# Optimization experiments

Hardware: AMD Instinct MI355X
Metric: run time of the kernel (lower is better)

The kernel has to match this reference:

```python
import jax, jax.numpy as jnp
import numpy as np

NUM_BANDS = 64
LATENT = 256
HIDDEN = 512
G = 8
K = 1024
GD = LATENT // G  # 32
BETA = 0.25


def setup_inputs() -> dict:
    key = jax.random.key(0)
    ks = jax.random.split(key, 10)
    B, T = 16, 1000
    bands = jax.random.normal(ks[0], (B, T, NUM_BANDS), dtype=jnp.float32)
    s = 0.02
    enc_w1 = jax.random.normal(ks[1], (NUM_BANDS, HIDDEN), dtype=jnp.float32) * s
    enc_b1 = jnp.zeros((HIDDEN,), dtype=jnp.float32)
    enc_w2 = jax.random.normal(ks[2], (HIDDEN, LATENT), dtype=jnp.float32) * s
    enc_b2 = jnp.zeros((LATENT,), dtype=jnp.float32)
    codebooks = jax.random.normal(ks[3], (G, K, GD), dtype=jnp.float32) * 0.1
    dec_w1 = jax.random.normal(ks[4], (LATENT, HIDDEN), dtype=jnp.float32) * s
    dec_b1 = jnp.zeros((HIDDEN,), dtype=jnp.float32)
    dec_w2 = jax.random.normal(ks[5], (HIDDEN, NUM_BANDS), dtype=jnp.float32) * s
    dec_b2 = jnp.zeros((NUM_BANDS,), dtype=jnp.float32)
    return {
        "bands": bands,
        "enc_w1": enc_w1, "enc_b1": enc_b1, "enc_w2": enc_w2, "enc_b2": enc_b2,
        "codebooks": codebooks,
        "dec_w1": dec_w1, "dec_b1": dec_b1, "dec_w2": dec_w2, "dec_b2": dec_b2,
    }


def _mlp(x, w1, b1, w2, b2):
    # TimeDistributedMLP: Linear -> ReLU -> Linear applied on last dim
    return jax.nn.relu(x @ w1 + b1) @ w2 + b2


def reference(bands, enc_w1, enc_b1, enc_w2, enc_b2, codebooks,
              dec_w1, dec_b1, dec_w2, dec_b2):
    B, T, _ = bands.shape
    z_e = _mlp(bands, enc_w1, enc_b1, enc_w2, enc_b2)  # (B,T,LATENT)

    # Grouped VQ over flattened frames
    parts = z_e.reshape(B * T, G, GD)                   # (N,G,gd)
    zn = jnp.sum(parts * parts, axis=-1)[:, :, None]    # (N,G,1)
    cn = jnp.sum(codebooks * codebooks, axis=-1)[None]  # (1,G,K)
    cross = jnp.einsum('ngd,gkd->ngk', parts, codebooks)
    dist = zn - 2.0 * cross + cn                        # (N,G,K)
    idx = jnp.argmin(dist, axis=-1)                     # (N,G) int
    z_q = codebooks[jnp.arange(G)[None, :], idx]        # (N,G,gd) gather

    # straight-through estimator
    z_q_st = parts + jax.lax.stop_gradient(z_q - parts)

    # per-group mean losses, summed over groups
    codebook_loss = jnp.sum(jnp.mean((jax.lax.stop_gradient(z_q) - parts) ** 2, axis=(0, 2)))
    commit_loss = jnp.sum(jnp.mean((z_q - jax.lax.stop_gradient(parts)) ** 2, axis=(0, 2)))
    vq_loss = BETA * (codebook_loss + commit_loss)  # epoch=None -> beta_eff = beta

    z_q_out = z_q_st.reshape(B, T, LATENT)
    idx_out = idx.reshape(B, T, G)
    bands_hat = _mlp(z_q_out, dec_w1, dec_b1, dec_w2, dec_b2)
    return (bands_hat, z_e, z_q_out, idx_out, vq_loss)
```

## Files before the change

kernel.cpp:

```cpp
#include <hip/hip_runtime.h>

#define NBANDS 64
#define LATENT 256
#define HIDDEN 512
#define GQ 8
#define KQ 1024
#define GD 32
#define NROWS 16000

#define OUT_BH   0
#define OUT_ZE   1024000
#define OUT_ZQ   5120000
#define OUT_IDX  9216000
#define OUT_LOSS 9344000

#define WS_H     0
#define WS_H2BF_F  0
#define WS_ZQB_F   4096000
#define WS_W1B_F   6144000
#define WS_W2B_F   6209536
#define WS_CN    8192000
#define WS_LOSS  8200192

typedef __attribute__((ext_vector_type(8))) short bf16x8;
typedef __attribute__((ext_vector_type(4))) float f32x4;

__device__ __forceinline__ unsigned short f2bf(float f) {
  unsigned u = __builtin_bit_cast(unsigned, f);
  unsigned r = u + 0x7FFFu + ((u >> 16) & 1u);
  return (unsigned short)(r >> 16);
}

__device__ __forceinline__ void g2l16(const float* g, float* l) {
  __builtin_amdgcn_global_load_lds(
      (const __attribute__((address_space(1))) unsigned int*)g,
      (__attribute__((address_space(3))) unsigned int*)l, 16, 0, 0);
}

template<int BN, int TM, int TN, int BK, bool RELU>
__global__ __launch_bounds__(256) void gemm_f32(
    const float* __restrict__ A, const float* __restrict__ B,
    const float* __restrict__ bias, float* __restrict__ C,
    int M, int N, int K) {
  constexpr int BM = 128;
  constexpr int NTX = BN / TN;
  constexpr int AF4 = BK / 8;
  constexpr int QPR = BN / 4;
  constexpr int BF4 = BK * BN / 1024;

  __shared__ float As[BK][BM + 8];
  __shared__ float Bs[BK][BN + 4];

  const int tid = threadIdx.x;
  const int tx = tid % NTX;
  const int ty = tid / NTX;
  const int row0 = blockIdx.y * BM;
  const int col0 = blockIdx.x * BN;

  const int arow = tid >> 1;
  const int akq  = (tid & 1) * (BK / 2);

  float acc[TM][TN] = {};

  for (int k0 = 0; k0 < K; k0 += BK) {
    float4 av[AF4], bv[BF4];
#pragma unroll
    for (int q = 0; q < AF4; ++q)
      av[q] = *reinterpret_cast<const float4*>(
          &A[(size_t)(row0 + arow) * K + k0 + akq + q * 4]);
#pragma unroll
    for (int t = 0; t < BF4; ++t) {
      const int qq = tid * BF4 + t;
      const int bk = qq / QPR, bn4 = qq % QPR;
      bv[t] = *reinterpret_cast<const float4*>(
          &B[(size_t)(k0 + bk) * N + col0 + bn4 * 4]);
    }
    __syncthreads();
#pragma unroll
    for (int q = 0; q < AF4; ++q) {
      As[akq + q * 4 + 0][arow] = av[q].x;
      As[akq + q * 4 + 1][arow] = av[q].y;
      As[akq + q * 4 + 2][arow] = av[q].z;
      As[akq + q * 4 + 3][arow] = av[q].w;
    }
#pragma unroll
    for (int t = 0; t < BF4; ++t) {
      const int qq = tid * BF4 + t;
      const int bk = qq / QPR, bn4 = qq % QPR;
      *reinterpret_cast<float4*>(&Bs[bk][bn4 * 4]) = bv[t];
    }
    __syncthreads();

#pragma unroll
    for (int kk = 0; kk < BK; ++kk) {
      float a[TM], b[TN];
#pragma unroll
      for (int q = 0; q < TM / 4; ++q) {
        float4 v = *reinterpret_cast<const float4*>(&As[kk][ty * TM + q * 4]);
        a[q * 4 + 0] = v.x; a[q * 4 + 1] = v.y;
        a[q * 4 + 2] = v.z; a[q * 4 + 3] = v.w;
      }
#pragma unroll
      for (int q = 0; q < TN / 4; ++q) {
        float4 v = *reinterpret_cast<const float4*>(&Bs[kk][tx * TN + q * 4]);
        b[q * 4 + 0] = v.x; b[q * 4 + 1] = v.y;
        b[q * 4 + 2] = v.z; b[q * 4 + 3] = v.w;
      }
#pragma unroll
      for (int i = 0; i < TM; ++i)
#pragma unroll
        for (int j = 0; j < TN; ++j)
          acc[i][j] = fmaf(a[i], b[j], acc[i][j]);
    }
  }

  float bb[TN];
#pragma unroll
  for (int q = 0; q < TN / 4; ++q) {
    float4 v = *reinterpret_cast<const float4*>(&bias[col0 + tx * TN + q * 4]);
    bb[q * 4 + 0] = v.x; bb[q * 4 + 1] = v.y;
    bb[q * 4 + 2] = v.z; bb[q * 4 + 3] = v.w;
  }
#pragma unroll
  for (int i = 0; i < TM; ++i) {
    const int r = row0 + ty * TM + i;
#pragma unroll
    for (int q = 0; q < TN / 4; ++q) {
      float4 v;
      float* vp = &v.x;
#pragma unroll
      for (int j = 0; j < 4; ++j) {
        float t = acc[i][q * 4 + j] + bb[q * 4 + j];
        if (RELU) t = fmaxf(t, 0.0f);
        vp[j] = t;
      }
      *reinterpret_cast<float4*>(&C[(size_t)r * N + col0 + tx * TN + q * 4]) = v;
    }
  }
}

template<int WM, bool OUT_BF16, bool DO_LOSS>
__global__ __launch_bounds__(256) void gemm_bf16_mfma(
    const unsigned short* __restrict__ A, const unsigned short* __restrict__ BT,
    const float* __restrict__ bias, void* __restrict__ Cout,
    int M, int N, int K,
    const float* __restrict__ loss_acc, float* __restrict__ loss_out) {
  constexpr int BM = 4 * WM;
  constexpr int MT = WM / 16;

  __shared__ unsigned short As[BM][40];
  __shared__ unsigned short Bs[64][40];

  const int tid  = threadIdx.x;
  const int wave = tid >> 6;
  const int lane = tid & 63;
  const int quad = lane >> 4;
  const int l16  = lane & 15;
  const int row0 = blockIdx.y * BM;
  const int col0 = blockIdx.x * 64;

  if (DO_LOSS && blockIdx.x == 0 && blockIdx.y == 0 && tid == 0)
    loss_out[0] = 0.5f * loss_acc[0] / (float)((size_t)NROWS * GD);

  f32x4 acc[MT][4];
#pragma unroll
  for (int mt = 0; mt < MT; ++mt)
#pragma unroll
    for (int nt = 0; nt < 4; ++nt) acc[mt][nt] = (f32x4){0.f, 0.f, 0.f, 0.f};

  for (int k0 = 0; k0 < K; k0 += 32) {
    __syncthreads();
    if constexpr (BM == 128) {
      const int r = tid >> 1, seg = (tid & 1) * 16;
      const uint4* src = reinterpret_cast<const uint4*>(
          &A[(size_t)(row0 + r) * K + k0 + seg]);
      uint4* dst = reinterpret_cast<uint4*>(&As[r][seg]);
      dst[0] = src[0]; dst[1] = src[1];
    } else {
      const int r = tid >> 2, seg = (tid & 3) * 8;
      *reinterpret_cast<uint4*>(&As[r][seg]) =
          *reinterpret_cast<const uint4*>(&A[(size_t)(row0 + r) * K + k0 + seg]);
    }
    {
      const int n = tid >> 2, kc = (tid & 3) * 8;
      *reinterpret_cast<uint4*>(&Bs[n][kc]) =
          *reinterpret_cast<const uint4*>(&BT[(size_t)(col0 + n) * K + k0 + kc]);
    }
    __syncthreads();

    bf16x8 af[MT], bf[4];
#pragma unroll
    for (int mt = 0; mt < MT; ++mt)
      af[mt] = *reinterpret_cast<const bf16x8*>(
          &As[wave * WM + mt * 16 + l16][quad * 8]);
#pragma unroll
    for (int nt = 0; nt < 4; ++nt)
      bf[nt] = *reinterpret_cast<const bf16x8*>(&Bs[nt * 16 + l16][quad * 8]);
#pragma unroll
    for (int mt = 0; mt < MT; ++mt)
#pragma unroll
      for (int nt = 0; nt < 4; ++nt)
        acc[mt][nt] = __builtin_amdgcn_mfma_f32_16x16x32_bf16(
            af[mt], bf[nt], acc[mt][nt], 0, 0, 0);
  }

#pragma unroll
  for (int mt = 0; mt < MT; ++mt)
#pragma unroll
    for (int nt = 0; nt < 4; ++nt) {
      const int col = col0 + nt * 16 + l16;
      const float bv = bias[col];
#pragma unroll
      for (int r = 0; r < 4; ++r) {
        const int grow = row0 + wave * WM + mt * 16 + quad * 4 + r;
        float v = acc[mt][nt][r] + bv;
        if constexpr (OUT_BF16) {
          v = fmaxf(v, 0.0f);
          ((unsigned short*)Cout)[(size_t)grow * N + col] = f2bf(v);
        } else {
          ((float*)Cout)[(size_t)grow * N + col] = v;
        }
      }
    }
}

__global__ void prep_cn(const float* __restrict__ cb, float* __restrict__ cn,
                        float* __restrict__ loss_acc) {
  const int i = blockIdx.x * 256 + threadIdx.x;
  if (i == 0) loss_acc[0] = 0.0f;
  if (i < GQ * KQ) {
    const float* c = cb + (size_t)i * GD;
    float s = 0.0f;
#pragma unroll
    for (int d = 0; d < GD; ++d) s = fmaf(c[d], c[d], s);
    cn[i] = s;
  }
}

__global__ void prep_wT(const float* __restrict__ w1, const float* __restrict__ w2,
                        unsigned short* __restrict__ w1bT,
                        unsigned short* __restrict__ w2bT) {
  const int t = blockIdx.x * 256 + threadIdx.x;
  if (t < 16384) {
    const int n = t >> 5, k0 = (t & 31) * 8;
    alignas(16) unsigned short o[8];
#pragma unroll
    for (int q = 0; q < 8; ++q) o[q] = f2bf(w1[(size_t)(k0 + q) * HIDDEN + n]);
    *reinterpret_cast<uint4*>(&w1bT[(size_t)n * LATENT + k0]) =
        *reinterpret_cast<const uint4*>(o);
  } else if (t < 20480) {
    const int u = t - 16384;
    const int n = u >> 6, k0 = (u & 63) * 8;
    alignas(16) unsigned short o[8];
#pragma unroll
    for (int q = 0; q < 8; ++q) o[q] = f2bf(w2[(size_t)(k0 + q) * NBANDS + n]);
    *reinterpret_cast<uint4*>(&w2bT[(size_t)n * HIDDEN + k0]) =
        *reinterpret_cast<const uint4*>(o);
  }
}

#define VQ_ROWS 128
#define VQ_CHUNK 128
#define VQ_NCHUNK (KQ / VQ_CHUNK)
#define ZPAD 36

__global__ __launch_bounds__(256) void vq_kernel(
    const float* __restrict__ z_e, const float* __restrict__ cb,
    const float* __restrict__ cn, float* __restrict__ z_q,
    unsigned short* __restrict__ zqb,
    float* __restrict__ idx_out, float* __restrict__ loss_acc) {
  const int g    = blockIdx.y;
  const int row0 = blockIdx.x * VQ_ROWS;
  const int tid  = threadIdx.x;
  const int tx   = tid & 15;
  const int ty   = tid >> 4;

  __shared__ float smem[VQ_ROWS * ZPAD + 2 * VQ_CHUNK * GD];
  float* zs  = smem;
  float* cbF = smem + VQ_ROWS * ZPAD;

  const float* cbg = cb + (size_t)g * KQ * GD;
  const float* cng = cn + (size_t)g * KQ;

  {
    const float* src = cbg;
    float* dst = cbF;
#pragma unroll
    for (int q4 = 0; q4 < 4; ++q4) {
      const int s = q4 * 256 + tid;
      const int r = s >> 3;
      const int q = (s & 7) ^ (r & 7);
      g2l16(src + r * GD + q * 4, dst + s * 4);
    }
  }

  {
    const int r   = tid >> 1;
    const int off = (tid & 1) << 4;
    const int key = ((r >> 3) & 3) << 2;
    const float4* src = reinterpret_cast<const float4*>(
        &z_e[(size_t)(row0 + r) * LATENT + g * GD + off]);
#pragma unroll
    for (int q = 0; q < 4; ++q)
      *reinterpret_cast<float4*>(&zs[r * ZPAD + ((off + q * 4) ^ key)]) = src[q];
  }

  const int akey = (ty & 3) << 2;
  const int bkey = tx & 7;

  float best[8];
  int   bidx[8];
#pragma unroll
  for (int i = 0; i < 8; ++i) { best[i] = 3.0e38f; bidx[i] = 0; }

  for (int ch = 0; ch < VQ_NCHUNK; ++ch) {
    __syncthreads();

    if (ch + 1 < VQ_NCHUNK) {
      const float* src = cbg + (size_t)(ch + 1) * VQ_CHUNK * GD;
      float* dst = cbF + ((ch + 1) & 1) * (VQ_CHUNK * GD);
#pragma unroll
      for (int q4 = 0; q4 < 4; ++q4) {
        const int s = q4 * 256 + tid;
        const int r = s >> 3;
        const int q = (s & 7) ^ (r & 7);
        g2l16(src + r * GD + q * 4, dst + s * 4);
      }
    }

    const float* cbuf = cbF + (ch & 1) * (VQ_CHUNK * GD);

    float acc[8][8];
#pragma unroll
    for (int i = 0; i < 8; ++i)
#pragma unroll
      for (int j = 0; j < 8; ++j) acc[i][j] = 0.0f;

#pragma unroll 2
    for (int d0 = 0; d0 < GD; d0 += 4) {
      float4 a[8], b[8];
#pragma unroll
      for (int s = 0; s < 8; ++s)
        a[s] = *reinterpret_cast<const float4*>(
            &zs[(ty * 8 + s) * ZPAD + (d0 ^ akey)]);
      const int bq = ((d0 >> 2) ^ bkey) << 2;
#pragma unroll
      for (int j = 0; j < 8; ++j)
        b[j] = *reinterpret_cast<const float4*>(
            &cbuf[(j * 16 + tx) * GD + bq]);
#pragma unroll
      for (int i = 0; i < 8; ++i)
#pragma unroll
        for (int j = 0; j < 8; ++j) {
          float t = acc[i][j];
          t = fmaf(a[i].x, b[j].x, t);
          t = fmaf(a[i].y, b[j].y, t);
          t = fmaf(a[i].z, b[j].z, t);
          t = fmaf(a[i].w, b[j].w, t);
          acc[i][j] = t;
        }
    }

#pragma unroll
    for (int j = 0; j < 8; ++j) {
      const int k = ch * VQ_CHUNK + j * 16 + tx;
      const float cnv = cng[k];
#pragma unroll
      for (int i = 0; i < 8; ++i) {
        const float dist = fmaf(-2.0f, acc[i][j], cnv);
        if (dist < best[i]) { best[i] = dist; bidx[i] = k; }
      }
    }
  }

  __syncthreads();
  float* m_d = cbF;
  int*   m_i = reinterpret_cast<int*>(cbF + 16 * 129);
  float* red = cbF + 2 * 16 * 129 + 32;
#pragma unroll
  for (int i = 0; i < 8; ++i) {
    m_d[tx * 129 + ty * 8 + i] = best[i];
    m_i[tx * 129 + ty * 8 + i] = bidx[i];
  }
  __syncthreads();

  float sse_part = 0.0f;
  if (tid < VQ_ROWS) {
    const int row = tid;
    const int rkey = ((row >> 3) & 3) << 2;
    float mb = m_d[row];
    int   mi = m_i[row];
#pragma unroll
    for (int t = 1; t < 16; ++t) {
      const float v = m_d[t * 129 + row];
      const int  ix = m_i[t * 129 + row];
      if (v < mb || (v == mb && ix < mi)) { mb = v; mi = ix; }
    }

    const float* c = cbg + (size_t)mi * GD;
    float cw[GD];
#pragma unroll
    for (int q = 0; q < 8; ++q) {
      float4 v = *reinterpret_cast<const float4*>(&c[q * 4]);
      cw[q * 4 + 0] = v.x; cw[q * 4 + 1] = v.y;
      cw[q * 4 + 2] = v.z; cw[q * 4 + 3] = v.w;
    }
    float sse = 0.0f;
#pragma unroll
    for (int d = 0; d < GD; ++d) {
      const float diff = cw[d] - zs[row * ZPAD + (d ^ rkey)];
      sse = fmaf(diff, diff, sse);
    }
    float4* zq = reinterpret_cast<float4*>(
        &z_q[(size_t)(row0 + row) * LATENT + g * GD]);
#pragma unroll
    for (int q = 0; q < 8; ++q)
      zq[q] = make_float4(cw[q * 4], cw[q * 4 + 1], cw[q * 4 + 2], cw[q * 4 + 3]);

    alignas(16) unsigned short zb[GD];
#pragma unroll
    for (int d = 0; d < GD; ++d) zb[d] = f2bf(cw[d]);
    uint4* dstb = reinterpret_cast<uint4*>(
        zqb + (size_t)(row0 + row) * LATENT + g * GD);
    const uint4* srcb = reinterpret_cast<const uint4*>(zb);
#pragma unroll
    for (int q = 0; q < 4; ++q) dstb[q] = srcb[q];

    idx_out[(size_t)(row0 + row) * GQ + g] = (float)mi;
    sse_part = sse;
  }

  if (tid < VQ_ROWS) red[tid] = sse_part;
  __syncthreads();
  if (tid < 64) {
    float s = red[tid] + red[tid + 64];
#pragma unroll
    for (int off = 32; off > 0; off >>= 1)
      s += __shfl_down(s, off, 64);
    if (tid == 0) atomicAdd(loss_acc, s);
  }
}

extern "C" void kernel_launch(void* const* d_in, const int* in_sizes, int n_in,
                              void* d_out, int out_size, void* d_ws, size_t ws_size,
                              hipStream_t stream) {
  const float* bands  = (const float*)d_in[0];
  const float* enc_w1 = (const float*)d_in[1];
  const float* enc_b1 = (const float*)d_in[2];
  const float* enc_w2 = (const float*)d_in[3];
  const float* enc_b2 = (const float*)d_in[4];
  const float* cbooks = (const float*)d_in[5];
  const float* dec_w1 = (const float*)d_in[6];
  const float* dec_b1 = (const float*)d_in[7];
  const float* dec_w2 = (const float*)d_in[8];
  const float* dec_b2 = (const float*)d_in[9];

  float* out = (float*)d_out;
  float* ws  = (float*)d_ws;

  float* bands_hat = out + OUT_BH;
  float* z_e       = out + OUT_ZE;
  float* z_q       = out + OUT_ZQ;
  float* idx_f     = out + OUT_IDX;
  float* loss_out  = out + OUT_LOSS;

  float* H        = ws + WS_H;
  float* cn       = ws + WS_CN;
  float* loss_acc = ws + WS_LOSS;
  unsigned short* h2bf = (unsigned short*)(ws + WS_H2BF_F);
  unsigned short* zqb  = (unsigned short*)(ws + WS_ZQB_F);
  unsigned short* w1bT = (unsigned short*)(ws + WS_W1B_F);
  unsigned short* w2bT = (unsigned short*)(ws + WS_W2B_F);

  prep_cn<<<dim3(32), dim3(256), 0, stream>>>(cbooks, cn, loss_acc);

  gemm_f32<128, 8, 8, 16, true ><<<dim3(HIDDEN / 128, NROWS / 128), dim3(256), 0, stream>>>(
      bands, enc_w1, enc_b1, H, NROWS, HIDDEN, NBANDS);
  gemm_f32<64, 4, 8, 32, false><<<dim3(LATENT / 64, NROWS / 128), dim3(256), 0, stream>>>(
      H, enc_w2, enc_b2, z_e, NROWS, LATENT, HIDDEN);

  prep_wT<<<dim3(80), dim3(256), 0, stream>>>(dec_w1, dec_w2, w1bT, w2bT);

  vq_kernel<<<dim3(NROWS / VQ_ROWS, GQ), dim3(256), 0, stream>>>(
      z_e, cbooks, cn, z_q, zqb, idx_f, loss_acc);

  gemm_bf16_mfma<32, true, true ><<<dim3(HIDDEN / 64, NROWS / 128), dim3(256), 0, stream>>>(
      zqb, w1bT, dec_b1, (void*)h2bf, NROWS, HIDDEN, LATENT, loss_acc, loss_out);
  gemm_bf16_mfma<16, false, false><<<dim3(NBANDS / 64, NROWS / 64), dim3(256), 0, stream>>>(
      h2bf, w2bT, dec_b2, (void*)bands_hat, NROWS, NBANDS, HIDDEN, loss_acc, loss_out);
}
```

Measured before the change: 328.4 us.

## Compute VQ distances with bf16x3 split MFMA instead of FP32 FMA

Replaces the FP32 SIMT VQ distance kernel with an MFMA kernel. Both the latent vectors and the codebook are split into three bf16 parts (high, mid, low), and six bf16 MFMA products approximate the FP32 dot product. Codebook norms are pre-scaled by -0.5 so the argmin turns into an argmax seeded through the accumulator. Codebook splits are made in the prep kernel, and codebook tiles are read straight from global memory with no LDS staging. The risk is small precision differences that could flip argmin ties, plus extra global traffic for the codebook reads.

```diff
diff --git a/kernel.cpp b/kernel.cpp
--- a/kernel.cpp
+++ b/kernel.cpp
@@ -19,6 +19,9 @@
 #define WS_ZQB_F   4096000
 #define WS_W1B_F   6144000
 #define WS_W2B_F   6209536
+#define WS_CBH_F   6240000
+#define WS_CBM_F   6400000
+#define WS_CBL_F   6560000
 #define WS_CN    8192000
 #define WS_LOSS  8200192
 
@@ -31,10 +34,17 @@
   return (unsigned short)(r >> 16);
 }
 
-__device__ __forceinline__ void g2l16(const float* g, float* l) {
-  __builtin_amdgcn_global_load_lds(
-      (const __attribute__((address_space(1))) unsigned int*)g,
-      (__attribute__((address_space(3))) unsigned int*)l, 16, 0, 0);
+__device__ __forceinline__ float bf2f(unsigned short h) {
+  return __builtin_bit_cast(float, ((unsigned)h) << 16);
+}
+
+__device__ __forceinline__ void split3(float x, unsigned short& h,
+                                       unsigned short& m, unsigned short& l) {
+  h = f2bf(x);
+  const float r1 = x - bf2f(h);
+  m = f2bf(r1);
+  const float r2 = r1 - bf2f(m);
+  l = f2bf(r2);
 }
 
 template<int BN, int TM, int TN, int BK, bool RELU>
@@ -233,13 +243,17 @@
     float s = 0.0f;
 #pragma unroll
     for (int d = 0; d < GD; ++d) s = fmaf(c[d], c[d], s);
-    cn[i] = s;
+    cn[i] = -0.5f * s;
   }
 }
 
 __global__ void prep_wT(const float* __restrict__ w1, const float* __restrict__ w2,
+                        const float* __restrict__ cbk,
                         unsigned short* __restrict__ w1bT,
-                        unsigned short* __restrict__ w2bT) {
+                        unsigned short* __restrict__ w2bT,
+                        unsigned short* __restrict__ cbh,
+                        unsigned short* __restrict__ cbm,
+                        unsigned short* __restrict__ cbl) {
   const int t = blockIdx.x * 256 + threadIdx.x;
   if (t < 16384) {
     const int n = t >> 5, k0 = (t & 31) * 8;
@@ -256,189 +270,123 @@
     for (int q = 0; q < 8; ++q) o[q] = f2bf(w2[(size_t)(k0 + q) * NBANDS + n]);
     *reinterpret_cast<uint4*>(&w2bT[(size_t)n * HIDDEN + k0]) =
         *reinterpret_cast<const uint4*>(o);
-  }
-}
-
-#define VQ_ROWS 128
-#define VQ_CHUNK 128
-#define VQ_NCHUNK (KQ / VQ_CHUNK)
-#define ZPAD 36
-
-__global__ __launch_bounds__(256) void vq_kernel(
+  } else if (t < 53248) {
+    const int e0 = (t - 20480) * 8;
+    alignas(16) unsigned short oh[8], om[8], ol[8];
+#pragma unroll
+    for (int q = 0; q < 8; ++q) split3(cbk[e0 + q], oh[q], om[q], ol[q]);
+    *reinterpret_cast<uint4*>(&cbh[e0]) = *reinterpret_cast<const uint4*>(oh);
+    *reinterpret_cast<uint4*>(&cbm[e0]) = *reinterpret_cast<const uint4*>(om);
+    *reinterpret_cast<uint4*>(&cbl[e0]) = *reinterpret_cast<const uint4*>(ol);
+  }
+}
+
+__global__ __launch_bounds__(256) void vq_mfma(
     const float* __restrict__ z_e, const float* __restrict__ cb,
-    const float* __restrict__ cn, float* __restrict__ z_q,
-    unsigned short* __restrict__ zqb,
+    const float* __restrict__ cnh,
+    const unsigned short* __restrict__ cbh,
+    const unsigned short* __restrict__ cbm,
+    const unsigned short* __restrict__ cbl,
+    float* __restrict__ z_q, unsigned short* __restrict__ zqb,
     float* __restrict__ idx_out, float* __restrict__ loss_acc) {
   const int g    = blockIdx.y;
-  const int row0 = blockIdx.x * VQ_ROWS;
+  const int row0 = blockIdx.x * 128;
   const int tid  = threadIdx.x;
-  const int tx   = tid & 15;
-  const int ty   = tid >> 4;
-
-  __shared__ float smem[VQ_ROWS * ZPAD + 2 * VQ_CHUNK * GD];
-  float* zs  = smem;
-  float* cbF = smem + VQ_ROWS * ZPAD;
-
-  const float* cbg = cb + (size_t)g * KQ * GD;
-  const float* cng = cn + (size_t)g * KQ;
-
-  {
-    const float* src = cbg;
-    float* dst = cbF;
-#pragma unroll
-    for (int q4 = 0; q4 < 4; ++q4) {
-      const int s = q4 * 256 + tid;
-      const int r = s >> 3;
-      const int q = (s & 7) ^ (r & 7);
-      g2l16(src + r * GD + q * 4, dst + s * 4);
-    }
-  }
-
-  {
-    const int r   = tid >> 1;
-    const int off = (tid & 1) << 4;
-    const int key = ((r >> 3) & 3) << 2;
-    const float4* src = reinterpret_cast<const float4*>(
-        &z_e[(size_t)(row0 + r) * LATENT + g * GD + off]);
-#pragma unroll
-    for (int q = 0; q < 4; ++q)
-      *reinterpret_cast<float4*>(&zs[r * ZPAD + ((off + q * 4) ^ key)]) = src[q];
-  }
-
-  const int akey = (ty & 3) << 2;
-  const int bkey = tx & 7;
+  const int wave = tid >> 6;
+  const int lane = tid & 63;
+  const int quad = lane >> 4;
+  const int l16  = lane & 15;
+
+  bf16x8 ah[2], am[2], al[2];
+#pragma unroll
+  for (int mt = 0; mt < 2; ++mt) {
+    const float* zp = &z_e[(size_t)(row0 + wave * 32 + mt * 16 + l16) * LATENT
+                           + g * GD + quad * 8];
+    const float4 x0 = *reinterpret_cast<const float4*>(zp);
+    const float4 x1 = *reinterpret_cast<const float4*>(zp + 4);
+    const float xv[8] = {x0.x, x0.y, x0.z, x0.w, x1.x, x1.y, x1.z, x1.w};
+    bf16x8 vh, vm, vl;
+#pragma unroll
+    for (int j = 0; j < 8; ++j) {
+      unsigned short sh, sm, sl;
+      split3(xv[j], sh, sm, sl);
+      vh[j] = (short)sh; vm[j] = (short)sm; vl[j] = (short)sl;
+    }
+    ah[mt] = vh; am[mt] = vm; al[mt] = vl;
+  }
+
+  const size_t cb0 = (size_t)g * KQ * GD;
+  const float* cng = cnh + g * KQ;
 
   float best[8];
   int   bidx[8];
 #pragma unroll
-  for (int i = 0; i < 8; ++i) { best[i] = 3.0e38f; bidx[i] = 0; }
-
-  for (int ch = 0; ch < VQ_NCHUNK; ++ch) {
-    __syncthreads();
-
-    if (ch + 1 < VQ_NCHUNK) {
-      const float* src = cbg + (size_t)(ch + 1) * VQ_CHUNK * GD;
-      float* dst = cbF + ((ch + 1) & 1) * (VQ_CHUNK * GD);
-#pragma unroll
-      for (int q4 = 0; q4 < 4; ++q4) {
-        const int s = q4 * 256 + tid;
-        const int r = s >> 3;
-        const int q = (s & 7) ^ (r & 7);
-        g2l16(src + r * GD + q * 4, dst + s * 4);
+  for (int i = 0; i < 8; ++i) { best[i] = -3.0e38f; bidx[i] = 0; }
+
+#pragma unroll 2
+  for (int ch = 0; ch < 16; ++ch) {
+#pragma unroll
+    for (int nt = 0; nt < 4; ++nt) {
+      const int code = ch * 64 + nt * 16 + l16;
+      const size_t cba = cb0 + (size_t)code * GD + quad * 8;
+      const bf16x8 bh = *reinterpret_cast<const bf16x8*>(&cbh[cba]);
+      const bf16x8 bm = *reinterpret_cast<const bf16x8*>(&cbm[cba]);
+      const bf16x8 bl = *reinterpret_cast<const bf16x8*>(&cbl[cba]);
+      const float c0 = cng[code];
+      f32x4 a0 = {c0, c0, c0, c0};
+      f32x4 a1 = a0;
+      a0 = __builtin_amdgcn_mfma_f32_16x16x32_bf16(ah[0], bh, a0, 0, 0, 0);
+      a1 = __builtin_amdgcn_mfma_f32_16x16x32_bf16(ah[1], bh, a1, 0, 0, 0);
+      a0 = __builtin_amdgcn_mfma_f32_16x16x32_bf16(ah[0], bm, a0, 0, 0, 0);
+      a1 = __builtin_amdgcn_mfma_f32_16x16x32_bf16(ah[1], bm, a1, 0, 0, 0);
+      a0 = __builtin_amdgcn_mfma_f32_16x16x32_bf16(am[0], bh, a0, 0, 0, 0);
+      a1 = __builtin_amdgcn_mfma_f32_16x16x32_bf16(am[1], bh, a1, 0, 0, 0);
+      a0 = __builtin_amdgcn_mfma_f32_16x16x32_bf16(ah[0], bl, a0, 0, 0, 0);
+      a1 = __builtin_amdgcn_mfma_f32_16x16x32_bf16(ah[1], bl, a1, 0, 0, 0);
+      a0 = __builtin_amdgcn_mfma_f32_16x16x32_bf16(am[0], bm, a0, 0, 0, 0);
+      a1 = __builtin_amdgcn_mfma_f32_16x16x32_bf16(am[1], bm, a1, 0, 0, 0);
+      a0 = __builtin_amdgcn_mfma_f32_16x16x32_bf16(al[0], bh, a0, 0, 0, 0);
+      a1 = __builtin_amdgcn_mfma_f32_16x16x32_bf16(al[1], bh, a1, 0, 0, 0);
+#pragma unroll
+      for (int r = 0; r < 4; ++r) {
+        if (a0[r] > best[r])     { best[r] = a0[r];     bidx[r] = code; }
+        if (a1[r] > best[4 + r]) { best[4 + r] = a1[r]; bidx[4 + r] = code; }
       }
     }
-
-    const float* cbuf = cbF + (ch & 1) * (VQ_CHUNK * GD);
-
-    float acc[8][8];
-#pragma unroll
-    for (int i = 0; i < 8; ++i)
-#pragma unroll
-      for (int j = 0; j < 8; ++j) acc[i][j] = 0.0f;
-
-#pragma unroll 2
-    for (int d0 = 0; d0 < GD; d0 += 4) {
-      float4 a[8], b[8];
-#pragma unroll
-      for (int s = 0; s < 8; ++s)
-        a[s] = *reinterpret_cast<const float4*>(
-            &zs[(ty * 8 + s) * ZPAD + (d0 ^ akey)]);
-      const int bq = ((d0 >> 2) ^ bkey) << 2;
-#pragma unroll
-      for (int j = 0; j < 8; ++j)
-        b[j] = *reinterpret_cast<const float4*>(
-            &cbuf[(j * 16 + tx) * GD + bq]);
-#pragma unroll
-      for (int i = 0; i < 8; ++i)
-#pragma unroll
-        for (int j = 0; j < 8; ++j) {
-          float t = acc[i][j];
-          t = fmaf(a[i].x, b[j].x, t);
-          t = fmaf(a[i].y, b[j].y, t);
-          t = fmaf(a[i].z, b[j].z, t);
-          t = fmaf(a[i].w, b[j].w, t);
-          acc[i][j] = t;
-        }
-    }
-
-#pragma unroll
-    for (int j = 0; j < 8; ++j) {
-      const int k = ch * VQ_CHUNK + j * 16 + tx;
-      const float cnv = cng[k];
-#pragma unroll
-      for (int i = 0; i < 8; ++i) {
-        const float dist = fmaf(-2.0f, acc[i][j], cnv);
-        if (dist < best[i]) { best[i] = dist; bidx[i] = k; }
-      }
-    }
-  }
-
-  __syncthreads();
-  float* m_d = cbF;
-  int*   m_i = reinterpret_cast<int*>(cbF + 16 * 129);
-  float* red = cbF + 2 * 16 * 129 + 32;
-#pragma unroll
-  for (int i = 0; i < 8; ++i) {
-    m_d[tx * 129 + ty * 8 + i] = best[i];
-    m_i[tx * 129 + ty * 8 + i] = bidx[i];
-  }
-  __syncthreads();
-
-  float sse_part = 0.0f;
-  if (tid < VQ_ROWS) {
-    const int row = tid;
-    const int rkey = ((row >> 3) & 3) << 2;
-    float mb = m_d[row];
-    int   mi = m_i[row];
-#pragma unroll
-    for (int t = 1; t < 16; ++t) {
-      const float v = m_d[t * 129 + row];
-      const int  ix = m_i[t * 129 + row];
-      if (v < mb || (v == mb && ix < mi)) { mb = v; mi = ix; }
-    }
-
-    const float* c = cbg + (size_t)mi * GD;
-    float cw[GD];
-#pragma unroll
-    for (int q = 0; q < 8; ++q) {
-      float4 v = *reinterpret_cast<const float4*>(&c[q * 4]);
-      cw[q * 4 + 0] = v.x; cw[q * 4 + 1] = v.y;
-      cw[q * 4 + 2] = v.z; cw[q * 4 + 3] = v.w;
-    }
-    float sse = 0.0f;
-#pragma unroll
-    for (int d = 0; d < GD; ++d) {
-      const float diff = cw[d] - zs[row * ZPAD + (d ^ rkey)];
-      sse = fmaf(diff, diff, sse);
-    }
-    float4* zq = reinterpret_cast<float4*>(
-        &z_q[(size_t)(row0 + row) * LATENT + g * GD]);
-#pragma unroll
-    for (int q = 0; q < 8; ++q)
-      zq[q] = make_float4(cw[q * 4], cw[q * 4 + 1], cw[q * 4 + 2], cw[q * 4 + 3]);
-
-    alignas(16) unsigned short zb[GD];
-#pragma unroll
-    for (int d = 0; d < GD; ++d) zb[d] = f2bf(cw[d]);
-    uint4* dstb = reinterpret_cast<uint4*>(
-        zqb + (size_t)(row0 + row) * LATENT + g * GD);
-    const uint4* srcb = reinterpret_cast<const uint4*>(zb);
-#pragma unroll
-    for (int q = 0; q < 4; ++q) dstb[q] = srcb[q];
-
-    idx_out[(size_t)(row0 + row) * GQ + g] = (float)mi;
-    sse_part = sse;
-  }
-
-  if (tid < VQ_ROWS) red[tid] = sse_part;
-  __syncthreads();
-  if (tid < 64) {
-    float s = red[tid] + red[tid + 64];
-#pragma unroll
-    for (int off = 32; off > 0; off >>= 1)
-      s += __shfl_down(s, off, 64);
-    if (tid == 0) atomicAdd(loss_acc, s);
-  }
+  }
+
+  float sse_local = 0.0f;
+#pragma unroll
+  for (int s8 = 0; s8 < 8; ++s8) {
+    float mb = best[s8];
+    int   mi = bidx[s8];
+#pragma unroll
+    for (int m = 1; m < 16; m <<= 1) {
+      const float ov = __shfl_xor(mb, m, 64);
+      const int   oi = __shfl_xor(mi, m, 64);
+      if (ov > mb || (ov == mb && oi < mi)) { mb = ov; mi = oi; }
+    }
+    const int mt  = s8 >> 2;
+    const int r   = s8 & 3;
+    const int row = row0 + wave * 32 + mt * 16 + quad * 4 + r;
+    const float2 cw = *reinterpret_cast<const float2*>(
+        &cb[cb0 + (size_t)mi * GD + 2 * l16]);
+    const float2 zv = *reinterpret_cast<const float2*>(
+        &z_e[(size_t)row * LATENT + g * GD + 2 * l16]);
+    const float d0 = cw.x - zv.x;
+    const float d1 = cw.y - zv.y;
+    sse_local = fmaf(d0, d0, fmaf(d1, d1, sse_local));
+    *reinterpret_cast<float2*>(
+        &z_q[(size_t)row * LATENT + g * GD + 2 * l16]) = cw;
+    const unsigned pz = (unsigned)f2bf(cw.x) | ((unsigned)f2bf(cw.y) << 16);
+    *reinterpret_cast<unsigned*>(
+        &zqb[(size_t)row * LATENT + g * GD + 2 * l16]) = pz;
+    if (l16 == 0) idx_out[(size_t)row * GQ + g] = (float)mi;
+  }
+
+#pragma unroll
+  for (int m = 1; m < 64; m <<= 1) sse_local += __shfl_xor(sse_local, m, 64);
+  if (lane == 0) atomicAdd(loss_acc, sse_local);
 }
 
 extern "C" void kernel_launch(void* const* d_in, const int* in_sizes, int n_in,
@@ -471,6 +419,9 @@
   unsigned short* zqb  = (unsigned short*)(ws + WS_ZQB_F);
   unsigned short* w1bT = (unsigned short*)(ws + WS_W1B_F);
   unsigned short* w2bT = (unsigned short*)(ws + WS_W2B_F);
+  unsigned short* cbh  = (unsigned short*)(ws + WS_CBH_F);
+  unsigned short* cbm  = (unsigned short*)(ws + WS_CBM_F);
+  unsigned short* cbl  = (unsigned short*)(ws + WS_CBL_F);
 
   prep_cn<<<dim3(32), dim3(256), 0, stream>>>(cbooks, cn, loss_acc);
 
@@ -479,10 +430,11 @@
   gemm_f32<64, 4, 8, 32, false><<<dim3(LATENT / 64, NROWS / 128), dim3(256), 0, stream>>>(
       H, enc_w2, enc_b2, z_e, NROWS, LATENT, HIDDEN);
 
-  prep_wT<<<dim3(80), dim3(256), 0, stream>>>(dec_w1, dec_w2, w1bT, w2bT);
-
-  vq_kernel<<<dim3(NROWS / VQ_ROWS, GQ), dim3(256), 0, stream>>>(
-      z_e, cbooks, cn, z_q, zqb, idx_f, loss_acc);
+  prep_wT<<<dim3(208), dim3(256), 0, stream>>>(
+      dec_w1, dec_w2, cbooks, w1bT, w2bT, cbh, cbm, cbl);
+
+  vq_mfma<<<dim3(NROWS / 128, GQ), dim3(256), 0, stream>>>(
+      z_e, cbooks, cn, cbh, cbm, cbl, z_q, zqb, idx_f, loss_acc);
 
   gemm_bf16_mfma<32, true, true ><<<dim3(HIDDEN / 64, NROWS / 128), dim3(256), 0, stream>>>(
       zqb, w1bT, dec_b1, (void*)h2bf, NROWS, HIDDEN, LATENT, loss_acc, loss_out);
```

Result: faster. 304.7 us (-7.2%).
